# Optimization experiments

Measured on AMD Instinct MI355X. Metric: run time of the kernel, lower is better.

The kernel has to match this reference:

```python
import jax, jax.numpy as jnp
import numpy as np

EPS = 1e-15


def _trace(t):
    return jnp.einsum('bii->b', t)


def _ortho_loss(ss, k):
    n = jnp.linalg.norm(ss, axis=(-1, -2), keepdims=True)
    diff = ss / n - jnp.eye(k, dtype=ss.dtype) / np.float32(np.sqrt(k))
    return jnp.mean(jnp.linalg.norm(diff, axis=(-1, -2)))


def _mincut_terms(s, adj):
    out_adj = jnp.einsum('bnk,bnm,bml->bkl', s, adj, s)
    d_flat = adj.sum(-1)  # degrees [B,N]
    num = _trace(out_adj)
    den = _trace(jnp.einsum('bnk,bn,bnl->bkl', s, d_flat, s)) + EPS
    return out_adj, num, den, d_flat


def dense_mincut_rewiring(x, adj, s, mask):
    k = s.shape[-1]  # 2
    m = mask[..., None].astype(x.dtype)
    s = jax.nn.softmax(s, axis=-1) * m
    _, num, den, _ = _mincut_terms(s, adj)
    mincut_loss = -jnp.mean(num / den)
    ortho_loss = _ortho_loss(jnp.einsum('bnk,bnl->bkl', s, s), k)
    # laplacian derivative of spectral gap wrt A_uv: (f_u - f_v)^2, f = soft bipartition
    f = s[..., 0]
    dlam = (f[:, :, None] - f[:, None, :]) ** 2
    return adj * (1.0 - dlam), mincut_loss, ortho_loss


def dense_CT_rewiring(x, adj, s, mask):
    k = s.shape[-1]
    m = mask[..., None].astype(x.dtype)
    s = jax.nn.softmax(s, axis=-1) * m
    d_flat = adj.sum(-1)
    sds = _trace(jnp.einsum('bnk,bn,bnl->bkl', s, d_flat, s))
    sas = _trace(jnp.einsum('bnk,bnm,bml->bkl', s, adj, s))
    den = _trace(jnp.einsum('bnk,bnl->bkl', s, s)) + EPS
    ct_loss = jnp.mean((sds - sas) / den)  # tr(Z^T L Z) / tr(Z^T Z)
    ortho_loss = _ortho_loss(jnp.einsum('bnk,bnl->bkl', s, s), k)
    # pairwise CT distances ||z_u - z_v|| / vol(G), sparsified by A
    sq = (s * s).sum(-1)
    d2 = sq[:, :, None] + sq[:, None, :] - 2.0 * jnp.einsum('bnk,bmk->bnm', s, s)
    ct_dist = jnp.sqrt(jnp.maximum(d2, 0.0) + 1e-12)
    vol = d_flat.sum(-1)
    new_adj = (ct_dist / (vol[:, None, None] + EPS)) * adj
    return new_adj, ct_loss, ortho_loss


def dense_mincut_pool(x, adj, s, mask):
    k = s.shape[-1]
    m = mask[..., None].astype(x.dtype)
    s = jax.nn.softmax(s, axis=-1) * m
    x = x * m
    out = jnp.einsum('bnk,bnf->bkf', s, x)
    out_adj, num, den, _ = _mincut_terms(s, adj)
    mincut_loss = -jnp.mean(num / den)
    ortho_loss = _ortho_loss(jnp.einsum('bnk,bnl->bkl', s, s), k)
    out_adj = out_adj * (1.0 - jnp.eye(k, dtype=adj.dtype))  # zero diagonal
    d = jnp.sqrt(out_adj.sum(-1)) + EPS  # [B,k]
    out_adj = out_adj / d[:, None, :] / d[:, :, None]
    return out, out_adj, mincut_loss, ortho_loss


def _dgc(x, adj, w_rel, b_rel, w_root):
    # DenseGraphConv(aggr='add'): lin_rel(A @ x) + lin_root(x)
    return jnp.matmul(adj, x) @ w_rel + b_rel + x @ w_root


def setup_inputs() -> dict:
    B, N, IN, H, KC, OUT, KMC = 16, 1024, 128, 32, 32, 10, 16
    keys = iter(jax.random.split(jax.random.key(0), 48))

    def lin(fin, fout):
        lim = float(1.0 / np.sqrt(fin))
        return (jax.random.uniform(next(keys), (fin, fout), jnp.float32, -lim, lim),
                jax.random.uniform(next(keys), (fout,), jnp.float32, -lim, lim))

    x = jax.random.normal(next(keys), (B, N, IN), jnp.float32)
    u = jax.random.uniform(next(keys), (B, N, N), jnp.float32)
    a = (u < 0.0156).astype(jnp.float32)  # avg degree ~16
    adj = jnp.maximum(a, jnp.swapaxes(a, 1, 2)) * (1.0 - jnp.eye(N, dtype=jnp.float32))
    mask = jnp.ones((B, N), dtype=bool)
    W1, b1 = lin(IN, H)
    Wrw, brw = lin(H, 2)
    Wg_rel, bg = lin(H, H); Wg_root, _ = lin(H, H)
    Wmcg, bmcg = lin(H, KMC)
    W2g_rel, b2g = lin(H, H); W2g_root, _ = lin(H, H)
    Wct, bct = lin(H, KC)
    Wc_rel, bc = lin(H, H); Wc_root, _ = lin(H, H)
    Wmcc, bmcc = lin(H, KMC)
    Wcat, bcat = lin(2 * H, H)
    W2, b2 = lin(H, H)
    W3, b3 = lin(H, OUT)
    return dict(x=x, adj=adj, mask=mask, W1=W1, b1=b1, Wrw=Wrw, brw=brw,
                Wg_rel=Wg_rel, bg=bg, Wg_root=Wg_root, Wmcg=Wmcg, bmcg=bmcg,
                W2g_rel=W2g_rel, b2g=b2g, W2g_root=W2g_root, Wct=Wct, bct=bct,
                Wc_rel=Wc_rel, bc=bc, Wc_root=Wc_root, Wmcc=Wmcc, bmcc=bmcc,
                Wcat=Wcat, bcat=bcat, W2=W2, b2=b2, W3=W3, b3=b3)


def reference(x, adj, mask, W1, b1, Wrw, brw, Wg_rel, bg, Wg_root, Wmcg, bmcg,
              W2g_rel, b2g, W2g_root, Wct, bct, Wc_rel, bc, Wc_root, Wmcc, bmcc,
              Wcat, bcat, W2, b2, W3, b3):
    x = x @ W1 + b1
    # GAP branch
    adj_gap, mc_rw, ol_rw = dense_mincut_rewiring(x, adj, x @ Wrw + brw, mask)
    x_gap = _dgc(x, adj_gap, Wg_rel, bg, Wg_root)
    x_gap, adj_gap, mc1, ol1 = dense_mincut_pool(x_gap, adj_gap, x_gap @ Wmcg + bmcg, mask)
    x_gap = _dgc(x_gap, adj_gap, W2g_rel, b2g, W2g_root)
    # CT branch
    adj_ct, ct_loss, ol_ct = dense_CT_rewiring(x, adj, x @ Wct + bct, mask)
    x_ct = _dgc(x, adj_ct, Wc_rel, bc, Wc_root)
    x_ct, adj_ct, mc2, ol2 = dense_mincut_pool(x_ct, adj_ct, x_ct @ Wmcc + bmcc, mask)
    x_ct = _dgc(x_ct, adj_ct, W2g_rel, b2g, W2g_root)  # source reuses self.conv2gap here
    h = jax.nn.relu(jnp.concatenate([x_gap, x_ct], axis=2) @ Wcat + bcat).sum(axis=1)
    h = jax.nn.relu(h @ W2 + b2)
    logits = h @ W3 + b3
    main_loss = mc_rw + ct_loss + mc1 + mc2
    ortho_loss = ol_rw + ol_ct + ol1 + ol2
    return (jax.nn.log_softmax(logits, axis=-1), main_loss, ortho_loss)
```

## Files before the change

### kernel.cpp

```cpp
#include <hip/hip_runtime.h>
#include <math.h>

#define BB   16
#define NNODE 1024
#define INF_ 128
#define HH   32
#define KMC  16
#define CAP  128
#define EPS15 1e-15f

typedef float v4f __attribute__((ext_vector_type(4)));

#define OFF_X      0
#define OFF_SRW    524288
#define OFF_SQCT   557056
#define OFF_SCT    573440
#define OFF_D      1097728
#define OFF_NUMRW  1114112
#define OFF_SAS    1130496
#define OFF_DGAP   1146880
#define OFF_DCT    1163264
#define OFF_XGAP   2228224
#define OFF_XCT    2752512
#define OFF_S2G    3276800
#define OFF_S2C    3538944
#define OFF_FROB   4325376
#define OFF_VOL    4325888
#define OFF_OUTG   4326032
#define OFF_OUTC   4334224
#define OFF_G2G    4342416
#define OFF_G2C    4346512
#define OFF_OAG    4350608
#define OFF_OAC    4354704
#define OFF_ENNZ   4358800
#define OFF_EIDX   4375184
#define OFF_EWG    5423760
#define OFF_EWC    7520912
#define OFF_PACK   9618064
#define OFF_BSUM   9683600

__device__ __forceinline__ float wave_sum(float v) {
#pragma unroll
  for (int off = 32; off >= 1; off >>= 1) v += __shfl_xor(v, off, 64);
  return v;
}

__device__ __forceinline__ void wave_sum4(float& a, float& b, float& c, float& d) {
#pragma unroll
  for (int off = 32; off >= 1; off >>= 1) {
    a += __shfl_xor(a, off, 64);
    b += __shfl_xor(b, off, 64);
    c += __shfl_xor(c, off, 64);
    d += __shfl_xor(d, off, 64);
  }
}

__device__ __forceinline__ float blk_sum(float v, float* sred, int tid) {
  v = wave_sum(v);
  __syncthreads();
  if ((tid & 63) == 0) sred[tid >> 6] = v;
  __syncthreads();
  return sred[0] + sred[1] + sred[2] + sred[3];
}

__device__ __forceinline__ void blk_sum5(float* v, float (*sm)[4], int tid) {
  int w = tid >> 6, lane = tid & 63;
#pragma unroll
  for (int i = 0; i < 5; i++) {
#pragma unroll
    for (int off = 32; off >= 1; off >>= 1) v[i] += __shfl_xor(v[i], off, 64);
  }
  if (lane == 0) {
#pragma unroll
    for (int i = 0; i < 5; i++) sm[i][w] = v[i];
  }
  __syncthreads();
#pragma unroll
  for (int i = 0; i < 5; i++) v[i] = sm[i][0] + sm[i][1] + sm[i][2] + sm[i][3];
}

__global__ __launch_bounds__(256) void k_fused0(
    const float* __restrict__ adj, const float* __restrict__ x,
    const float* __restrict__ W1, const float* __restrict__ b1,
    const float* __restrict__ Wrw, const float* __restrict__ brw,
    const float* __restrict__ Wct, const float* __restrict__ bct,
    float* __restrict__ ws)
{
  __shared__ __align__(16) float sW1[INF_*HH];
  __shared__ __align__(16) float sWct[HH*HH];
  __shared__ float sWrw[HH*2];
  __shared__ float sb1[HH], sbct[HH], sbrw[2];
  __shared__ __align__(16) float sx[8*INF_];
  __shared__ float sX[8*HH];
  __shared__ unsigned int s_e32[4][4][CAP/2];
  int tid = threadIdx.x;
  if (blockIdx.x < 1024) {
    int w = tid >> 6, lane = tid & 63;
    int row0 = blockIdx.x * 16 + w * 4;
    v4f v[16];
#pragma unroll
    for (int rr = 0; rr < 4; rr++) {
      const v4f* ar = (const v4f*)(adj + (size_t)(row0 + rr) * NNODE);
#pragma unroll
      for (int it = 0; it < 4; it++)
        v[rr*4 + it] = __builtin_nontemporal_load(&ar[it*64 + lane]);
    }
#pragma unroll
    for (int rr = 0; rr < 4; rr++) {
      int row = row0 + rr;
      int c = 0;
#pragma unroll
      for (int it = 0; it < 4; it++) {
        v4f a4 = v[rr*4 + it];
        c += (a4.x != 0.f) + (a4.y != 0.f) + (a4.z != 0.f) + (a4.w != 0.f);
      }
      int p = c;
#pragma unroll
      for (int off = 1; off < 64; off <<= 1) {
        int t = __shfl_up(p, off, 64);
        if (lane >= off) p += t;
      }
      int excl = p - c;
      int total = __shfl(p, 63, 64);
      unsigned short* es = (unsigned short*)s_e32[w][rr];
      int pos = excl;
#pragma unroll
      for (int it = 0; it < 4; it++) {
        v4f a4 = v[rr*4 + it];
        int m0 = it*256 + lane*4;
        if (a4.x != 0.f) { if (pos < CAP) es[pos] = (unsigned short)(m0+0); pos++; }
        if (a4.y != 0.f) { if (pos < CAP) es[pos] = (unsigned short)(m0+1); pos++; }
        if (a4.z != 0.f) { if (pos < CAP) es[pos] = (unsigned short)(m0+2); pos++; }
        if (a4.w != 0.f) { if (pos < CAP) es[pos] = (unsigned short)(m0+3); pos++; }
      }
      int nnzc = total < CAP ? total : CAP;
      __syncthreads();
      unsigned int* dst = (unsigned int*)((unsigned short*)(ws + OFF_EIDX) + (size_t)row*CAP);
      int n32 = (nnzc + 1) >> 1;
      if (lane < n32) dst[lane] = s_e32[w][rr][lane];
      if (lane == 0) {
        ((int*)(ws + OFF_ENNZ))[row] = nnzc;
        ws[OFF_D + row] = (float)total;
      }
    }
  } else {
    for (int i = tid; i < INF_*HH/4; i += 256)
      ((float4*)sW1)[i] = ((const float4*)W1)[i];
    ((float4*)sWct)[tid] = ((const float4*)Wct)[tid];
    if (tid < HH*2) sWrw[tid] = Wrw[tid];
    if (tid < HH) { sb1[tid] = b1[tid]; sbct[tid] = bct[tid]; }
    if (tid < 2) sbrw[tid] = brw[tid];
    size_t row0 = (size_t)(blockIdx.x - 1024) * 8;
    ((float4*)sx)[tid] = ((const float4*)(x + row0 * INF_))[tid];
    __syncthreads();
    int r = tid >> 5, h = tid & 31;
    float acc = sb1[h];
#pragma unroll 8
    for (int k = 0; k < INF_; k++) acc += sx[r*INF_ + k] * sW1[k*HH + h];
    size_t row = row0 + r;
    ws[OFF_X + row*HH + h] = acc;
    sX[r*HH + h] = acc;
    __syncthreads();
    float sraw = sbct[h];
#pragma unroll
    for (int k = 0; k < HH; k++) sraw += sX[r*HH + k] * sWct[k*HH + h];
    float mx = sraw;
#pragma unroll
    for (int off = 16; off >= 1; off >>= 1) mx = fmaxf(mx, __shfl_xor(mx, off, 32));
    float e = __expf(sraw - mx);
    float sum = e;
#pragma unroll
    for (int off = 16; off >= 1; off >>= 1) sum += __shfl_xor(sum, off, 32);
    float sv = e / sum;
    ws[OFF_SCT + row*HH + h] = sv;
    float sq = sv * sv;
#pragma unroll
    for (int off = 16; off >= 1; off >>= 1) sq += __shfl_xor(sq, off, 32);
    float xv = sX[r*HH + h];
    float t0 = xv * sWrw[h*2 + 0];
    float t1 = xv * sWrw[h*2 + 1];
#pragma unroll
    for (int off = 16; off >= 1; off >>= 1) { t0 += __shfl_xor(t0, off, 32); t1 += __shfl_xor(t1, off, 32); }
    if (h == 0) {
      ws[OFF_SQCT + row] = sq;
      float r0 = t0 + sbrw[0], r1 = t1 + sbrw[1];
      float m2 = fmaxf(r0, r1);
      float e0 = __expf(r0 - m2), e1 = __expf(r1 - m2);
      float inv = 1.0f / (e0 + e1);
      float s0 = e0*inv, s1 = e1*inv;
      ((float2*)(ws + OFF_SRW))[row] = make_float2(s0, s1);
      ((float4*)(ws + OFF_PACK))[row] = make_float4(s0, s1, sq, 0.f);
    }
  }
}

__global__ __launch_bounds__(256) void k_edgefeat(
    const float* __restrict__ Wg_rel, const float* __restrict__ bg, const float* __restrict__ Wg_root,
    const float* __restrict__ Wc_rel, const float* __restrict__ bc, const float* __restrict__ Wc_root,
    const float* __restrict__ Wmcg, const float* __restrict__ bmcg,
    const float* __restrict__ Wmcc, const float* __restrict__ bmcc,
    float* __restrict__ out, float* __restrict__ ws)
{
  __shared__ unsigned short s_m[4][CAP];
  __shared__ float s_wg[4][CAP];
  __shared__ float s_wc[4][CAP];
  __shared__ float sp[8][32];
  __shared__ float sred[4];
  __shared__ __align__(16) float sWgrel[HH*HH], sWgroot[HH*HH], sWcrel[HH*HH], sWcroot[HH*HH];
  __shared__ float sbg[HH], sbc[HH];
  __shared__ float sYg[4*HH], sYc[4*HH], sXr[4*HH], sxg[4*HH], sxc[4*HH];
  int tid = threadIdx.x;
  if (blockIdx.x < 4096) {
    int xcd = blockIdx.x & 7;
    int idx = blockIdx.x >> 3;
    int b = xcd*2 + (idx >> 8);
    int chunk = idx & 255;
    int base4 = b*NNODE + chunk*4;
    ((float4*)sWgrel)[tid]  = ((const float4*)Wg_rel)[tid];
    ((float4*)sWgroot)[tid] = ((const float4*)Wg_root)[tid];
    ((float4*)sWcrel)[tid]  = ((const float4*)Wc_rel)[tid];
    ((float4*)sWcroot)[tid] = ((const float4*)Wc_root)[tid];
    if (tid < HH)  { sbg[tid] = bg[tid]; sbc[tid] = bc[tid]; }
    if (tid < 128) sXr[tid] = ws[OFF_X + (size_t)base4*HH + tid];
    float vp = 0.f;
#pragma unroll
    for (int i = 0; i < 4; i++) vp += ws[OFF_D + (size_t)b*NNODE + tid + i*256];

    const float* X = ws + OFF_X;
    const float2* srw = (const float2*)(ws + OFF_SRW);
    const float* sqct = ws + OFF_SQCT;
    const float* sct = ws + OFF_SCT;
    const float4* pack = (const float4*)(ws + OFF_PACK) + (size_t)b*NNODE;
    int w = tid >> 6, lane = tid & 63;
    int tm = lane & 3;
    int row = base4 + w;
    int nnz = ((const int*)(ws + OFF_ENNZ))[row];
    const unsigned short* eidx = (const unsigned short*)(ws + OFF_EIDX) + (size_t)row*CAP;
    const float4* cn4 = (const float4*)(sct + (size_t)row * HH);
    float4 c0 = cn4[tm*2], c1 = cn4[tm*2 + 1];
    float2 srwn = srw[row];
    float f_n = srwn.x;
    float sq_n = sqct[row];
    float numrw_p = 0.f, sas_p = 0.f, dg_p = 0.f, dc_p = 0.f;
    for (int e = (lane >> 2); e < nnz; e += 16) {
      int m = eidx[e];
      const float4* cm4 = (const float4*)(sct + ((size_t)b*NNODE + m) * HH);
      float4 d0 = cm4[tm*2], d1 = cm4[tm*2 + 1];
      float dot = c0.x*d0.x + c0.y*d0.y + c0.z*d0.z + c0.w*d0.w
                + c1.x*d1.x + c1.y*d1.y + c1.z*d1.z + c1.w*d1.w;
      dot += __shfl_xor(dot, 1, 64);
      dot += __shfl_xor(dot, 2, 64);
      float4 pk = pack[m];
      numrw_p += srwn.x*pk.x + srwn.y*pk.y;
      float df = f_n - pk.x;
      float wg = 1.0f - df*df;
      float d2 = sq_n + pk.z - 2.0f*dot;
      float wc = sqrtf(fmaxf(d2, 0.0f) + 1e-12f);
      sas_p += dot;
      dg_p += wg;
      dc_p += wc;
      if (tm == 0) {
        s_m[w][e] = (unsigned short)m;
        s_wg[w][e] = wg;
        s_wc[w][e] = wc;
        size_t eo = (size_t)row*CAP + e;
        ws[OFF_EWG + eo] = wg;
        ws[OFF_EWC + eo] = wc;
      }
    }
    wave_sum4(numrw_p, sas_p, dg_p, dc_p);
    if (lane == 0) {
      ws[OFF_NUMRW + row] = numrw_p * 0.25f;
      ws[OFF_SAS + row] = sas_p * 0.25f;
      ws[OFF_DGAP + row] = dg_p * 0.25f;
      ws[OFF_DCT + row] = dc_p * 0.25f;
    }
    int eoff = lane >> 4, hp = lane & 15;
    float yg0 = 0.f, yg1 = 0.f, yc0 = 0.f, yc1 = 0.f;
    for (int e = eoff; e < nnz; e += 4) {
      int m = s_m[w][e];
      float wg = s_wg[w][e], wc = s_wc[w][e];
      float2 xv = ((const float2*)(X + ((size_t)b*NNODE + m)*HH))[hp];
      yg0 += wg*xv.x; yg1 += wg*xv.y;
      yc0 += wc*xv.x; yc1 += wc*xv.y;
    }
    yg0 += __shfl_xor(yg0, 16, 64); yg0 += __shfl_xor(yg0, 32, 64);
    yg1 += __shfl_xor(yg1, 16, 64); yg1 += __shfl_xor(yg1, 32, 64);
    yc0 += __shfl_xor(yc0, 16, 64); yc0 += __shfl_xor(yc0, 32, 64);
    yc1 += __shfl_xor(yc1, 16, 64); yc1 += __shfl_xor(yc1, 32, 64);
    if (eoff == 0) {
      sYg[w*HH + 2*hp] = yg0; sYg[w*HH + 2*hp + 1] = yg1;
      sYc[w*HH + 2*hp] = yc0; sYc[w*HH + 2*hp + 1] = yc1;
    }
    float vol = blk_sum(vp, sred, tid);
    float ivol = 1.0f / (vol + EPS15);
    {
      int r = tid >> 6;
      int h = (tid >> 1) & 31;
      int half = tid & 1;
      int kb = half * 16;
      float accg = 0.f, accg2 = 0.f, accc = 0.f, accc2 = 0.f;
#pragma unroll
      for (int kk = 0; kk < 16; kk++) {
        int k = kb + kk;
        float ygv = sYg[r*HH + k], Xv = sXr[r*HH + k], ycv = sYc[r*HH + k];
        accg  += ygv * sWgrel[k*HH + h];
        accg2 += Xv  * sWgroot[k*HH + h];
        accc  += ycv * sWcrel[k*HH + h];
        accc2 += Xv  * sWcroot[k*HH + h];
      }
      accg  += __shfl_xor(accg, 1, 64);
      accg2 += __shfl_xor(accg2, 1, 64);
      accc  += __shfl_xor(accc, 1, 64);
      accc2 += __shfl_xor(accc2, 1, 64);
      if (half == 0) {
        float xgv = sbg[h] + accg + accg2;
        float xcv = sbc[h] + ivol*accc + accc2;
        size_t rw = (size_t)base4 + r;
        ws[OFF_XGAP + rw*HH + h] = xgv;
        ws[OFF_XCT  + rw*HH + h] = xcv;
        sxg[r*HH + h] = xgv;
        sxc[r*HH + h] = xcv;
      }
    }
    __syncthreads();
    if (tid < 128) {
      int r = tid >> 5, h = tid & 31;
      int j = h & 15, halfsel = h >> 4;
      const float* sin_ = halfsel ? sxc : sxg;
      const float* sw = halfsel ? Wmcc : Wmcg;
      float raw = halfsel ? bmcc[j] : bmcg[j];
#pragma unroll
      for (int k = 0; k < HH; k++) raw += sin_[r*HH + k] * sw[k*KMC + j];
      float mx = raw;
#pragma unroll
      for (int off = 8; off >= 1; off >>= 1) mx = fmaxf(mx, __shfl_xor(mx, off, 16));
      float e = __expf(raw - mx);
      float sum = e;
#pragma unroll
      for (int off = 8; off >= 1; off >>= 1) sum += __shfl_xor(sum, off, 16);
      float sv = e / sum;
      size_t rw = (size_t)base4 + r;
      if (halfsel == 0) ws[OFF_S2G + rw*KMC + j] = sv;
      else              ws[OFF_S2C + rw*KMC + j] = sv;
    }
  } else if (blockIdx.x < 4608) {
    int blk = blockIdx.x - 4096;
    int xcd = blk & 7;
    int idx = blk >> 3;
    int b = xcd*2 + (idx >> 5);
    int i = idx & 31;
    const float* sct = ws + OFF_SCT + (size_t)b*NNODE*HH;
    int j = tid & 31, seg = tid >> 5;
    float acc = 0.f;
    for (int n = seg*128; n < seg*128 + 128; n++)
      acc += sct[n*HH + i] * sct[n*HH + j];
    sp[seg][j] = acc;
    __syncthreads();
    if (tid < 32) {
      float g = 0.f;
#pragma unroll
      for (int s = 0; s < 8; s++) g += sp[s][tid];
      float p = g * g;
#pragma unroll
      for (int off = 16; off >= 1; off >>= 1) p += __shfl_xor(p, off, 32);
      if (tid == 0) ws[OFF_FROB + b*32 + i] = p;
    }
  } else {
    int b = blockIdx.x - 4608;
    if (b == 0 && tid < 2) out[160 + tid] = 0.f;
    if (tid < 12) ws[OFF_BSUM + b*12 + tid] = 0.f;
    for (int i = tid; i < 2048; i += 256) ws[OFF_OUTG + b*2048 + i] = 0.f;
    float vp = 0.f;
    for (int n = tid; n < NNODE; n += 256) vp += ws[OFF_D + (size_t)b*NNODE + n];
    float vol = blk_sum(vp, sred, tid);
    if (tid == 0) ws[OFF_VOL + b] = vol;
  }
}

__global__ __launch_bounds__(512) void k_passred(float* __restrict__ ws)
{
  __shared__ float sg[32*16], sc[32*16], stg[32*16], stc[32*16];
  __shared__ float sxg[32*32], sxc[32*32];
  int b = blockIdx.x >> 5, chunk = blockIdx.x & 31;
  int tid = threadIdx.x;
  size_t n0 = (size_t)b * NNODE + chunk * 32;
  const float* pG  = ws + OFF_S2G  + n0 * KMC;
  const float* pC  = ws + OFF_S2C  + n0 * KMC;
  const float* pXG = ws + OFF_XGAP + n0 * HH;
  const float* pXC = ws + OFF_XCT  + n0 * HH;
  sg[tid] = pG[tid];
  sc[tid] = pC[tid];
  sxg[tid] = pXG[tid]; sxg[tid + 512] = pXG[tid + 512];
  sxc[tid] = pXC[tid]; sxc[tid + 512] = pXC[tid + 512];
  int w = tid >> 6, lane = tid & 63;
  int grp = lane >> 5;
  int sl  = (lane >> 4) & 1;
  int k   = lane & 15;
  const float* S2 = ws + (grp ? OFF_S2C : OFF_S2G) + (size_t)b * NNODE * KMC;
  float* sT = grp ? stc : stg;
#pragma unroll
  for (int i = 0; i < 4; i++) {
    int rr = w * 4 + i;
    size_t row = n0 + rr;
    int nnz = ((const int*)(ws + OFF_ENNZ))[row];
    const unsigned short* eidx = (const unsigned short*)(ws + OFF_EIDX) + row * CAP;
    const float* ew = ws + (grp ? OFF_EWC : OFF_EWG) + row * CAP;
    float acc = 0.f;
    int e = sl;
    for (; e + 2 < nnz; e += 4) {
      int m0 = eidx[e], m1 = eidx[e + 2];
      float w0 = ew[e], w1 = ew[e + 2];
      acc += w0 * S2[(size_t)m0 * KMC + k] + w1 * S2[(size_t)m1 * KMC + k];
    }
    if (e < nnz) acc += ew[e] * S2[(size_t)eidx[e] * KMC + k];
    acc += __shfl_xor(acc, 16, 32);
    if (sl == 0) sT[rr * 16 + k] = acc;
  }
  __syncthreads();
  int sub = tid >> 8, t = tid & 255;
  { int k0 = t >> 5, h0 = t & 31;
    float og0 = 0.f, og1 = 0.f, oc0 = 0.f, oc1 = 0.f;
#pragma unroll
    for (int i = 0; i < 16; i++) {
      int r = sub * 16 + i;
      float xgv = sxg[r*32 + h0], xcv = sxc[r*32 + h0];
      og0 += sg[r*16 + k0]     * xgv;
      og1 += sg[r*16 + k0 + 8] * xgv;
      oc0 += sc[r*16 + k0]     * xcv;
      oc1 += sc[r*16 + k0 + 8] * xcv;
    }
    atomicAdd(&ws[OFF_OUTG + b*512 + k0*32 + h0],     og0);
    atomicAdd(&ws[OFF_OUTG + b*512 + (k0+8)*32 + h0], og1);
    atomicAdd(&ws[OFF_OUTC + b*512 + k0*32 + h0],     oc0);
    atomicAdd(&ws[OFF_OUTC + b*512 + (k0+8)*32 + h0], oc1);
  }
  { int kk = t >> 4, l = t & 15;
    float gg = 0.f, gc = 0.f, ag = 0.f, ac = 0.f;
#pragma unroll
    for (int i = 0; i < 16; i++) {
      int r = sub * 16 + i;
      float sgk = sg[r*16 + kk], sck = sc[r*16 + kk];
      gg += sgk * sg [r*16 + l];
      gc += sck * sc [r*16 + l];
      ag += sgk * stg[r*16 + l];
      ac += sck * stc[r*16 + l];
    }
    atomicAdd(&ws[OFF_G2G + b*256 + t], gg);
    atomicAdd(&ws[OFF_G2C + b*256 + t], gc);
    atomicAdd(&ws[OFF_OAG + b*256 + t], ag);
    atomicAdd(&ws[OFF_OAC + b*256 + t], ac);
  }
  if (tid < 32) {
    size_t gn = n0 + tid;
    float ng = 0.f, nc = 0.f;
#pragma unroll
    for (int j = 0; j < KMC; j++) {
      float a = sg[tid*16 + j], c2 = sc[tid*16 + j];
      ng += a*a; nc += c2*c2;
    }
    float dgv = ws[OFF_DGAP + gn];
    float dcv = ws[OFF_DCT + gn];
    float d   = ws[OFF_D + gn];
    float2 s  = ((const float2*)(ws + OFF_SRW))[gn];
    float sq  = ws[OFF_SQCT + gn];
    float nmr = ws[OFF_NUMRW + gn];
    float sasv= ws[OFF_SAS + gn];
    float u0 = dgv*ng, u1 = dcv*nc, u2 = ng, u3 = nc;
    float u4 = d*(s.x*s.x + s.y*s.y), u5 = nmr, u6 = d*sq, u7 = sasv;
    float u8 = sq, u9 = s.x*s.x, u10 = s.x*s.y, u11 = s.y*s.y;
#pragma unroll
    for (int off = 16; off >= 1; off >>= 1) {
      u0 += __shfl_xor(u0, off, 32);  u1 += __shfl_xor(u1, off, 32);
      u2 += __shfl_xor(u2, off, 32);  u3 += __shfl_xor(u3, off, 32);
      u4 += __shfl_xor(u4, off, 32);  u5 += __shfl_xor(u5, off, 32);
      u6 += __shfl_xor(u6, off, 32);  u7 += __shfl_xor(u7, off, 32);
      u8 += __shfl_xor(u8, off, 32);  u9 += __shfl_xor(u9, off, 32);
      u10 += __shfl_xor(u10, off, 32); u11 += __shfl_xor(u11, off, 32);
    }
    if (tid == 0) {
      float* bs = ws + OFF_BSUM + b*12;
      atomicAdd(bs + 0, u0);  atomicAdd(bs + 1, u1);  atomicAdd(bs + 2, u2);
      atomicAdd(bs + 3, u3);  atomicAdd(bs + 4, u4);  atomicAdd(bs + 5, u5);
      atomicAdd(bs + 6, u6);  atomicAdd(bs + 7, u7);  atomicAdd(bs + 8, u8);
      atomicAdd(bs + 9, u9);  atomicAdd(bs + 10, u10); atomicAdd(bs + 11, u11);
    }
  }
}

__global__ __launch_bounds__(256) void k_batch2(
    const float* __restrict__ W2g_rel, const float* __restrict__ b2g, const float* __restrict__ W2g_root,
    const float* __restrict__ Wcat, const float* __restrict__ bcat,
    const float* __restrict__ W2, const float* __restrict__ b2,
    const float* __restrict__ W3, const float* __restrict__ b3,
    float* __restrict__ out, float* __restrict__ ws)
{
  __shared__ float sOAg[256], sOAc[256], sOutg[512], sOutc[512];
  __shared__ float sW2grel[1024], sW2groot[1024], sWcat[2048], sW2l[1024];
  __shared__ float sPg[512], sPc[512], sXg2[512], sXc2[512], sHt[512];
  __shared__ float sHs[32], sH2[32], sLg[16], sScal[2];
  __shared__ float sdkg[16], sdkc[16];
  __shared__ float smm[5][4];
  int b = blockIdx.x, tid = threadIdx.x;
  sOAg[tid] = ws[OFF_OAG + b*256 + tid];
  sOAc[tid] = ws[OFF_OAC + b*256 + tid];
  sOutg[tid]       = ws[OFF_OUTG + b*512 + tid];
  sOutg[tid + 256] = ws[OFF_OUTG + b*512 + tid + 256];
  sOutc[tid]       = ws[OFF_OUTC + b*512 + tid];
  sOutc[tid + 256] = ws[OFF_OUTC + b*512 + tid + 256];
  for (int i = tid; i < 1024; i += 256) { sW2grel[i] = W2g_rel[i]; sW2groot[i] = W2g_root[i]; sW2l[i] = W2[i]; }
  for (int i = tid; i < 2048; i += 256) sWcat[i] = Wcat[i];
  float v[5];
  v[0] = (tid < 32) ? ws[OFF_FROB + b*32 + tid] : 0.f;
  float gv = ws[OFF_G2G + b*256 + tid];
  float cv = ws[OFF_G2C + b*256 + tid];
  v[1] = gv*gv; v[2] = cv*cv;
  __syncthreads();
  v[3] = (tid < 16) ? sOAg[tid*17] : 0.f;
  v[4] = (tid < 16) ? sOAc[tid*17] : 0.f;
  blk_sum5(v, smm, tid);
  float frob2 = v[0], frobg2 = v[1], frobc2 = v[2], num1 = v[3], num2u = v[4];
  float vol = ws[OFF_VOL + b];
  float ivol = 1.0f / (vol + EPS15);
  if (tid == 0) {
    const float* bs = ws + OFF_BSUM + b*12;
    float den1 = bs[0], den2u = bs[1], trg = bs[2], trc = bs[3];
    float denrw = bs[4], num = bs[5], sds = bs[6], sas = bs[7], denct = bs[8];
    float g00 = bs[9], g01 = bs[10], g11 = bs[11];
    float mcrw = -num / (denrw + EPS15);
    float ctb  = (sds - sas) / (denct + EPS15);
    float nrw = sqrtf(g00*g00 + 2.f*g01*g01 + g11*g11);
    float olrw = sqrtf(fmaxf(2.f - 2.f*(g00 + g11)/(nrw*1.41421356237f), 0.f));
    float nct = sqrtf(frob2);
    float olct = sqrtf(fmaxf(2.f - 2.f*denct/(nct*5.65685424949f), 0.f));
    float mc1 = -num1 / (den1 + EPS15);
    float mc2 = -(num2u*ivol) / (den2u*ivol + EPS15);
    float ol1 = sqrtf(fmaxf(2.f - 2.f*trg/(sqrtf(frobg2)*4.f), 0.f));
    float ol2 = sqrtf(fmaxf(2.f - 2.f*trc/(sqrtf(frobc2)*4.f), 0.f));
    atomicAdd(out + 160, (mcrw + ctb + mc1 + mc2) * 0.0625f);
    atomicAdd(out + 161, (olrw + olct + ol1 + ol2) * 0.0625f);
  }
  sOAc[tid] *= ivol;
  __syncthreads();
  if (tid < 16) { sOAg[tid*17] = 0.f; sOAc[tid*17] = 0.f; }
  __syncthreads();
  if (tid < 16) {
    float rg = 0.f, rc = 0.f;
#pragma unroll
    for (int l = 0; l < 16; l++) { rg += sOAg[tid*16 + l]; rc += sOAc[tid*16 + l]; }
    sdkg[tid] = sqrtf(rg) + EPS15;
    sdkc[tid] = sqrtf(rc) + EPS15;
  }
  __syncthreads();
  { int k = tid >> 4, l = tid & 15;
    sOAg[tid] /= (sdkg[k]*sdkg[l]);
    sOAc[tid] /= (sdkc[k]*sdkc[l]); }
  __syncthreads();
  { int k = tid >> 5, h = tid & 31;
    float p0 = 0, p1 = 0, q0 = 0, q1 = 0;
#pragma unroll
    for (int l = 0; l < 16; l++) {
      p0 += sOAg[k*16 + l] * sOutg[l*32 + h];
      p1 += sOAg[(k+8)*16 + l] * sOutg[l*32 + h];
      q0 += sOAc[k*16 + l] * sOutc[l*32 + h];
      q1 += sOAc[(k+8)*16 + l] * sOutc[l*32 + h];
    }
    sPg[k*32 + h] = p0; sPg[(k+8)*32 + h] = p1;
    sPc[k*32 + h] = q0; sPc[(k+8)*32 + h] = q1;
  }
  __syncthreads();
  { int k = tid >> 5, h = tid & 31;
    float bb2 = b2g[h];
    float a0 = bb2, a1 = bb2, c0 = bb2, c1 = bb2;
#pragma unroll
    for (int q = 0; q < 32; q++) {
      float wr = sW2grel[q*32 + h], wo = sW2groot[q*32 + h];
      a0 += sPg[k*32 + q]*wr + sOutg[k*32 + q]*wo;
      a1 += sPg[(k+8)*32 + q]*wr + sOutg[(k+8)*32 + q]*wo;
      c0 += sPc[k*32 + q]*wr + sOutc[k*32 + q]*wo;
      c1 += sPc[(k+8)*32 + q]*wr + sOutc[(k+8)*32 + q]*wo;
    }
    sXg2[k*32 + h] = a0; sXg2[(k+8)*32 + h] = a1;
    sXc2[k*32 + h] = c0; sXc2[(k+8)*32 + h] = c1;
  }
  __syncthreads();
  { int k = tid >> 5, h = tid & 31;
    float bb = bcat[h];
    float t0 = bb, t1 = bb;
#pragma unroll
    for (int q = 0; q < 32; q++) {
      float w1v = sWcat[q*32 + h], w2v = sWcat[(q+32)*32 + h];
      t0 += sXg2[k*32 + q]*w1v + sXc2[k*32 + q]*w2v;
      t1 += sXg2[(k+8)*32 + q]*w1v + sXc2[(k+8)*32 + q]*w2v;
    }
    sHt[k*32 + h] = fmaxf(t0, 0.f);
    sHt[(k+8)*32 + h] = fmaxf(t1, 0.f);
  }
  __syncthreads();
  if (tid < 32) {
    float s = 0.f;
#pragma unroll
    for (int k = 0; k < 16; k++) s += sHt[k*32 + tid];
    sHs[tid] = s;
  }
  __syncthreads();
  if (tid < 32) {
    float a = b2[tid];
#pragma unroll
    for (int q = 0; q < 32; q++) a += sHs[q]*sW2l[q*32 + tid];
    sH2[tid] = fmaxf(a, 0.f);
  }
  __syncthreads();
  if (tid < 10) {
    float a = b3[tid];
#pragma unroll
    for (int q = 0; q < 32; q++) a += sH2[q]*W3[q*10 + tid];
    sLg[tid] = a;
  }
  __syncthreads();
  if (tid == 0) {
    float m = sLg[0];
    for (int o = 1; o < 10; o++) m = fmaxf(m, sLg[o]);
    float se = 0.f;
    for (int o = 0; o < 10; o++) se += __expf(sLg[o] - m);
    sScal[0] = m; sScal[1] = logf(se);
  }
  __syncthreads();
  if (tid < 10) out[b*10 + tid] = sLg[tid] - sScal[0] - sScal[1];
}

extern "C" void kernel_launch(void* const* d_in, const int* in_sizes, int n_in,
                              void* d_out, int out_size, void* d_ws, size_t ws_size,
                              hipStream_t stream)
{
  const float* x       = (const float*)d_in[0];
  const float* adj     = (const float*)d_in[1];
  const float* W1      = (const float*)d_in[3];
  const float* b1      = (const float*)d_in[4];
  const float* Wrw     = (const float*)d_in[5];
  const float* brw     = (const float*)d_in[6];
  const float* Wg_rel  = (const float*)d_in[7];
  const float* bg      = (const float*)d_in[8];
  const float* Wg_root = (const float*)d_in[9];
  const float* Wmcg    = (const float*)d_in[10];
  const float* bmcg    = (const float*)d_in[11];
  const float* W2g_rel = (const float*)d_in[12];
  const float* b2g     = (const float*)d_in[13];
  const float* W2g_root= (const float*)d_in[14];
  const float* Wct     = (const float*)d_in[15];
  const float* bct     = (const float*)d_in[16];
  const float* Wc_rel  = (const float*)d_in[17];
  const float* bc      = (const float*)d_in[18];
  const float* Wc_root = (const float*)d_in[19];
  const float* Wmcc    = (const float*)d_in[20];
  const float* bmcc    = (const float*)d_in[21];
  const float* Wcat    = (const float*)d_in[22];
  const float* bcat    = (const float*)d_in[23];
  const float* W2      = (const float*)d_in[24];
  const float* b2      = (const float*)d_in[25];
  const float* W3      = (const float*)d_in[26];
  const float* b3      = (const float*)d_in[27];
  float* out = (float*)d_out;
  float* ws  = (float*)d_ws;

  k_fused0<<<dim3(3072), dim3(256), 0, stream>>>(adj, x, W1, b1, Wrw, brw, Wct, bct, ws);
  k_edgefeat<<<dim3(4624), dim3(256), 0, stream>>>(Wg_rel, bg, Wg_root, Wc_rel, bc, Wc_root,
                                                   Wmcg, bmcg, Wmcc, bmcc, out, ws);
  k_passred<<<dim3(512), dim3(512), 0, stream>>>(ws);
  k_batch2<<<dim3(16), dim3(256), 0, stream>>>(W2g_rel, b2g, W2g_root, Wcat, bcat,
                                               W2, b2, W3, b3, out, ws);
}
```

Measured before the change: 252.9 us.

## Fuse neighbor feature aggregation into edge loop and restructure pass-reduce gather

```diff
diff --git a/kernel.cpp b/kernel.cpp
--- a/kernel.cpp
+++ b/kernel.cpp
@@ -55,6 +55,16 @@
   }
 }
 
+__device__ __forceinline__ void team_reduce_f4(float4& a) {
+#pragma unroll
+  for (int off = 4; off <= 32; off <<= 1) {
+    a.x += __shfl_xor(a.x, off, 64);
+    a.y += __shfl_xor(a.y, off, 64);
+    a.z += __shfl_xor(a.z, off, 64);
+    a.w += __shfl_xor(a.w, off, 64);
+  }
+}
+
 __device__ __forceinline__ float blk_sum(float v, float* sred, int tid) {
   v = wave_sum(v);
   __syncthreads();
@@ -201,14 +211,12 @@
     const float* __restrict__ Wmcc, const float* __restrict__ bmcc,
     float* __restrict__ out, float* __restrict__ ws)
 {
-  __shared__ unsigned short s_m[4][CAP];
-  __shared__ float s_wg[4][CAP];
-  __shared__ float s_wc[4][CAP];
   __shared__ float sp[8][32];
   __shared__ float sred[4];
   __shared__ __align__(16) float sWgrel[HH*HH], sWgroot[HH*HH], sWcrel[HH*HH], sWcroot[HH*HH];
   __shared__ float sbg[HH], sbc[HH];
-  __shared__ float sYg[4*HH], sYc[4*HH], sXr[4*HH], sxg[4*HH], sxc[4*HH];
+  __shared__ __align__(16) float sYg[4*HH], sYc[4*HH];
+  __shared__ float sXr[4*HH], sxg[4*HH], sxc[4*HH];
   int tid = threadIdx.x;
   if (blockIdx.x < 4096) {
     int xcd = blockIdx.x & 7;
@@ -242,15 +250,20 @@
     float f_n = srwn.x;
     float sq_n = sqct[row];
     float numrw_p = 0.f, sas_p = 0.f, dg_p = 0.f, dc_p = 0.f;
+    float4 yg0 = make_float4(0,0,0,0), yg1 = make_float4(0,0,0,0);
+    float4 yc0 = make_float4(0,0,0,0), yc1 = make_float4(0,0,0,0);
     for (int e = (lane >> 2); e < nnz; e += 16) {
       int m = eidx[e];
-      const float4* cm4 = (const float4*)(sct + ((size_t)b*NNODE + m) * HH);
+      size_t mo = ((size_t)b*NNODE + m);
+      const float4* cm4 = (const float4*)(sct + mo * HH);
+      const float4* xm4 = (const float4*)(X + mo * HH);
       float4 d0 = cm4[tm*2], d1 = cm4[tm*2 + 1];
+      float4 x0 = xm4[tm*2], x1 = xm4[tm*2 + 1];
+      float4 pk = pack[m];
       float dot = c0.x*d0.x + c0.y*d0.y + c0.z*d0.z + c0.w*d0.w
                 + c1.x*d1.x + c1.y*d1.y + c1.z*d1.z + c1.w*d1.w;
       dot += __shfl_xor(dot, 1, 64);
       dot += __shfl_xor(dot, 2, 64);
-      float4 pk = pack[m];
       numrw_p += srwn.x*pk.x + srwn.y*pk.y;
       float df = f_n - pk.x;
       float wg = 1.0f - df*df;
@@ -259,10 +272,11 @@
       sas_p += dot;
       dg_p += wg;
       dc_p += wc;
+      yg0.x += wg*x0.x; yg0.y += wg*x0.y; yg0.z += wg*x0.z; yg0.w += wg*x0.w;
+      yg1.x += wg*x1.x; yg1.y += wg*x1.y; yg1.z += wg*x1.z; yg1.w += wg*x1.w;
+      yc0.x += wc*x0.x; yc0.y += wc*x0.y; yc0.z += wc*x0.z; yc0.w += wc*x0.w;
+      yc1.x += wc*x1.x; yc1.y += wc*x1.y; yc1.z += wc*x1.z; yc1.w += wc*x1.w;
       if (tm == 0) {
-        s_m[w][e] = (unsigned short)m;
-        s_wg[w][e] = wg;
-        s_wc[w][e] = wc;
         size_t eo = (size_t)row*CAP + e;
         ws[OFF_EWG + eo] = wg;
         ws[OFF_EWC + eo] = wc;
@@ -275,22 +289,13 @@
       ws[OFF_DGAP + row] = dg_p * 0.25f;
       ws[OFF_DCT + row] = dc_p * 0.25f;
     }
-    int eoff = lane >> 4, hp = lane & 15;
-    float yg0 = 0.f, yg1 = 0.f, yc0 = 0.f, yc1 = 0.f;
-    for (int e = eoff; e < nnz; e += 4) {
-      int m = s_m[w][e];
-      float wg = s_wg[w][e], wc = s_wc[w][e];
-      float2 xv = ((const float2*)(X + ((size_t)b*NNODE + m)*HH))[hp];
-      yg0 += wg*xv.x; yg1 += wg*xv.y;
-      yc0 += wc*xv.x; yc1 += wc*xv.y;
-    }
-    yg0 += __shfl_xor(yg0, 16, 64); yg0 += __shfl_xor(yg0, 32, 64);
-    yg1 += __shfl_xor(yg1, 16, 64); yg1 += __shfl_xor(yg1, 32, 64);
-    yc0 += __shfl_xor(yc0, 16, 64); yc0 += __shfl_xor(yc0, 32, 64);
-    yc1 += __shfl_xor(yc1, 16, 64); yc1 += __shfl_xor(yc1, 32, 64);
-    if (eoff == 0) {
-      sYg[w*HH + 2*hp] = yg0; sYg[w*HH + 2*hp + 1] = yg1;
-      sYc[w*HH + 2*hp] = yc0; sYc[w*HH + 2*hp + 1] = yc1;
+    team_reduce_f4(yg0); team_reduce_f4(yg1);
+    team_reduce_f4(yc0); team_reduce_f4(yc1);
+    if (lane < 4) {
+      ((float4*)&sYg[w*HH + tm*8])[0] = yg0;
+      ((float4*)&sYg[w*HH + tm*8])[1] = yg1;
+      ((float4*)&sYc[w*HH + tm*8])[0] = yc0;
+      ((float4*)&sYc[w*HH + tm*8])[1] = yc1;
     }
     float vol = blk_sum(vp, sred, tid);
     float ivol = 1.0f / (vol + EPS15);
@@ -382,7 +387,10 @@
 {
   __shared__ float sg[32*16], sc[32*16], stg[32*16], stc[32*16];
   __shared__ float sxg[32*32], sxc[32*32];
-  int b = blockIdx.x >> 5, chunk = blockIdx.x & 31;
+  int xcd = blockIdx.x & 7;
+  int idx = blockIdx.x >> 3;
+  int b = xcd*2 + (idx >> 5);
+  int chunk = idx & 31;
   int tid = threadIdx.x;
   size_t n0 = (size_t)b * NNODE + chunk * 32;
   const float* pG  = ws + OFF_S2G  + n0 * KMC;
@@ -393,29 +401,31 @@
   sc[tid] = pC[tid];
   sxg[tid] = pXG[tid]; sxg[tid + 512] = pXG[tid + 512];
   sxc[tid] = pXC[tid]; sxc[tid + 512] = pXC[tid + 512];
-  int w = tid >> 6, lane = tid & 63;
-  int grp = lane >> 5;
-  int sl  = (lane >> 4) & 1;
-  int k   = lane & 15;
-  const float* S2 = ws + (grp ? OFF_S2C : OFF_S2G) + (size_t)b * NNODE * KMC;
-  float* sT = grp ? stc : stg;
-#pragma unroll
-  for (int i = 0; i < 4; i++) {
-    int rr = w * 4 + i;
-    size_t row = n0 + rr;
+  {
+    int r = tid >> 4, k = tid & 15;
+    size_t row = n0 + r;
     int nnz = ((const int*)(ws + OFF_ENNZ))[row];
     const unsigned short* eidx = (const unsigned short*)(ws + OFF_EIDX) + row * CAP;
-    const float* ew = ws + (grp ? OFF_EWC : OFF_EWG) + row * CAP;
-    float acc = 0.f;
-    int e = sl;
-    for (; e + 2 < nnz; e += 4) {
-      int m0 = eidx[e], m1 = eidx[e + 2];
-      float w0 = ew[e], w1 = ew[e + 2];
-      acc += w0 * S2[(size_t)m0 * KMC + k] + w1 * S2[(size_t)m1 * KMC + k];
-    }
-    if (e < nnz) acc += ew[e] * S2[(size_t)eidx[e] * KMC + k];
-    acc += __shfl_xor(acc, 16, 32);
-    if (sl == 0) sT[rr * 16 + k] = acc;
+    const float* ewg = ws + OFF_EWG + row * CAP;
+    const float* ewc = ws + OFF_EWC + row * CAP;
+    const float* S2G = ws + OFF_S2G + (size_t)b * NNODE * KMC;
+    const float* S2C = ws + OFF_S2C + (size_t)b * NNODE * KMC;
+    float ag = 0.f, ac = 0.f;
+    int e = 0;
+    for (; e + 1 < nnz; e += 2) {
+      int m0 = eidx[e], m1 = eidx[e + 1];
+      float g0 = ewg[e], g1 = ewg[e + 1];
+      float c0 = ewc[e], c1 = ewc[e + 1];
+      ag += g0 * S2G[(size_t)m0 * KMC + k] + g1 * S2G[(size_t)m1 * KMC + k];
+      ac += c0 * S2C[(size_t)m0 * KMC + k] + c1 * S2C[(size_t)m1 * KMC + k];
+    }
+    if (e < nnz) {
+      int m = eidx[e];
+      ag += ewg[e] * S2G[(size_t)m * KMC + k];
+      ac += ewc[e] * S2C[(size_t)m * KMC + k];
+    }
+    stg[r * 16 + k] = ag;
+    stc[r * 16 + k] = ac;
   }
   __syncthreads();
   int sub = tid >> 8, t = tid & 255;
```

New measurement: 248.0 us. No clear change (-1.9%).

## Remap passred blocks per XCD and share edge indices across both branches

Applied to the files above, without the earlier changes.

```diff
diff --git a/kernel.cpp b/kernel.cpp
--- a/kernel.cpp
+++ b/kernel.cpp
@@ -134,7 +134,6 @@
         if (a4.w != 0.f) { if (pos < CAP) es[pos] = (unsigned short)(m0+3); pos++; }
       }
       int nnzc = total < CAP ? total : CAP;
-      __syncthreads();
       unsigned int* dst = (unsigned int*)((unsigned short*)(ws + OFF_EIDX) + (size_t)row*CAP);
       int n32 = (nnzc + 1) >> 1;
       if (lane < n32) dst[lane] = s_e32[w][rr][lane];
@@ -382,7 +381,10 @@
 {
   __shared__ float sg[32*16], sc[32*16], stg[32*16], stc[32*16];
   __shared__ float sxg[32*32], sxc[32*32];
-  int b = blockIdx.x >> 5, chunk = blockIdx.x & 31;
+  int xcd = blockIdx.x & 7;
+  int idx = blockIdx.x >> 3;
+  int b = xcd*2 + (idx >> 5);
+  int chunk = idx & 31;
   int tid = threadIdx.x;
   size_t n0 = (size_t)b * NNODE + chunk * 32;
   const float* pG  = ws + OFF_S2G  + n0 * KMC;
@@ -393,29 +395,31 @@
   sc[tid] = pC[tid];
   sxg[tid] = pXG[tid]; sxg[tid + 512] = pXG[tid + 512];
   sxc[tid] = pXC[tid]; sxc[tid + 512] = pXC[tid + 512];
-  int w = tid >> 6, lane = tid & 63;
-  int grp = lane >> 5;
-  int sl  = (lane >> 4) & 1;
-  int k   = lane & 15;
-  const float* S2 = ws + (grp ? OFF_S2C : OFF_S2G) + (size_t)b * NNODE * KMC;
-  float* sT = grp ? stc : stg;
-#pragma unroll
-  for (int i = 0; i < 4; i++) {
-    int rr = w * 4 + i;
-    size_t row = n0 + rr;
+  {
+    int r = tid >> 4, k = tid & 15;
+    size_t row = n0 + r;
     int nnz = ((const int*)(ws + OFF_ENNZ))[row];
     const unsigned short* eidx = (const unsigned short*)(ws + OFF_EIDX) + row * CAP;
-    const float* ew = ws + (grp ? OFF_EWC : OFF_EWG) + row * CAP;
-    float acc = 0.f;
-    int e = sl;
-    for (; e + 2 < nnz; e += 4) {
-      int m0 = eidx[e], m1 = eidx[e + 2];
-      float w0 = ew[e], w1 = ew[e + 2];
-      acc += w0 * S2[(size_t)m0 * KMC + k] + w1 * S2[(size_t)m1 * KMC + k];
-    }
-    if (e < nnz) acc += ew[e] * S2[(size_t)eidx[e] * KMC + k];
-    acc += __shfl_xor(acc, 16, 32);
-    if (sl == 0) sT[rr * 16 + k] = acc;
+    const float* ewg = ws + OFF_EWG + row * CAP;
+    const float* ewc = ws + OFF_EWC + row * CAP;
+    const float* S2G = ws + OFF_S2G + (size_t)b * NNODE * KMC;
+    const float* S2C = ws + OFF_S2C + (size_t)b * NNODE * KMC;
+    float ag = 0.f, ac = 0.f;
+    int e = 0;
+    for (; e + 1 < nnz; e += 2) {
+      int m0 = eidx[e], m1 = eidx[e + 1];
+      float g0 = ewg[e], g1 = ewg[e + 1];
+      float c0 = ewc[e], c1 = ewc[e + 1];
+      ag += g0 * S2G[(size_t)m0 * KMC + k] + g1 * S2G[(size_t)m1 * KMC + k];
+      ac += c0 * S2C[(size_t)m0 * KMC + k] + c1 * S2C[(size_t)m1 * KMC + k];
+    }
+    if (e < nnz) {
+      int m = eidx[e];
+      ag += ewg[e] * S2G[(size_t)m * KMC + k];
+      ac += ewc[e] * S2C[(size_t)m * KMC + k];
+    }
+    stg[r * 16 + k] = ag;
+    stc[r * 16 + k] = ac;
   }
   __syncthreads();
   int sub = tid >> 8, t = tid & 255;
```

After: 243.0 us, median of 2. 3.9% less time.
